# Kernel tuning notes

Hardware: AMD Instinct MI355X
Metric: run time of the kernel (lower is better)

The kernel has to match this reference:

```python
import jax, jax.numpy as jnp
import numpy as np

DIM = 512
QK_DIM = 128
B, N = 4, 4096
LN_EPS = 1e-5


def setup_inputs() -> dict:
    key = jax.random.key(0)
    ks = jax.random.split(key, 4)
    x = jax.random.normal(ks[0], (B, N, DIM), dtype=jnp.float32)
    ln_w = jnp.ones((DIM,), jnp.float32)
    ln_b = jnp.zeros((DIM,), jnp.float32)
    # Linear(dim -> qk_dim): torch default kaiming-uniform; small uniform is fine
    lim = 1.0 / np.sqrt(DIM)
    w_qk = jax.random.uniform(ks[1], (QK_DIM, DIM), jnp.float32, -lim, lim)
    b_qk = jax.random.uniform(ks[2], (QK_DIM,), jnp.float32, -lim, lim)
    # OffsetScale: gamma ~ N(0, 0.02), beta = 0, heads=2 (q, k)
    gamma = 0.02 * jax.random.normal(ks[3], (2, QK_DIM), jnp.float32)
    beta = jnp.zeros((2, QK_DIM), jnp.float32)
    return {"x": x, "ln_w": ln_w, "ln_b": ln_b, "w_qk": w_qk, "b_qk": b_qk, "gamma": gamma, "beta": beta}


def reference(x, ln_w, ln_b, w_qk, b_qk, gamma, beta):
    n = x.shape[-2]
    # LayerNorm over last dim
    mu = jnp.mean(x, axis=-1, keepdims=True)
    var = jnp.mean((x - mu) ** 2, axis=-1, keepdims=True)
    normed = (x - mu) * jax.lax.rsqrt(var + LN_EPS) * ln_w + ln_b
    # Linear + SiLU -> [b, n, qk_dim]
    qk = jax.nn.silu(jnp.einsum('bnd,ed->bne', normed, w_qk) + b_qk)
    # OffsetScale, heads=2 -> q, k
    q = qk * gamma[0] + beta[0]
    k = qk * gamma[1] + beta[1]
    # relu^2 row-normalized attention, [b, n, n]
    sim = jnp.einsum('bid,bjd->bij', q, k) / jnp.sqrt(jnp.float32(n))
    attn = jnp.square(jax.nn.relu(sim))
    attn = attn / (jnp.sum(attn, axis=-1, keepdims=True) + 1e-6)
    return attn
```

## Files before the change

### kernel.cpp

```cpp
#include <hip/hip_runtime.h>

#define DIM 512
#define QKD 128
#define BATCH 4
#define SEQ 4096

typedef __attribute__((ext_vector_type(8)))  _Float16 f16x8;
typedef __attribute__((ext_vector_type(4)))  _Float16 f16x4;
typedef __attribute__((ext_vector_type(4)))  float    f32x4;
typedef __attribute__((ext_vector_type(16))) float    f32x16;

__global__ __launch_bounds__(256) void wcvt_kernel(
    const float* __restrict__ w, _Float16* __restrict__ w16)
{
    const int i = (blockIdx.x * 256 + threadIdx.x) * 4;
    const float4 v = *(const float4*)(w + i);
    f16x4 o;
    o[0] = (_Float16)v.x; o[1] = (_Float16)v.y;
    o[2] = (_Float16)v.z; o[3] = (_Float16)v.w;
    *(f16x4*)(w16 + i) = o;
}

__global__ __launch_bounds__(256) void ln_qk_kernel(
    const float* __restrict__ x,
    const float* __restrict__ ln_w,
    const float* __restrict__ ln_b,
    const _Float16* __restrict__ w16,
    const float* __restrict__ b_qk,
    const float* __restrict__ gamma,
    const float* __restrict__ beta,
    _Float16* __restrict__ q_h,
    _Float16* __restrict__ k_h)
{
    __shared__ _Float16 As[32][520];
    const int tid  = threadIdx.x;
    const int wave = tid >> 6;
    const int lane = tid & 63;
    const int row0 = blockIdx.x * 32;

    float lw[8], lb[8];
    {
        const float4* w4 = (const float4*)ln_w;
        const float4* b4 = (const float4*)ln_b;
        float4 w0 = w4[lane * 2], w1 = w4[lane * 2 + 1];
        float4 b0 = b4[lane * 2], b1 = b4[lane * 2 + 1];
        lw[0]=w0.x; lw[1]=w0.y; lw[2]=w0.z; lw[3]=w0.w;
        lw[4]=w1.x; lw[5]=w1.y; lw[6]=w1.z; lw[7]=w1.w;
        lb[0]=b0.x; lb[1]=b0.y; lb[2]=b0.z; lb[3]=b0.w;
        lb[4]=b1.x; lb[5]=b1.y; lb[6]=b1.z; lb[7]=b1.w;
    }

    for (int rr = 0; rr < 8; ++rr) {
        const int r = wave * 8 + rr;
        const float4* xr = (const float4*)(x + (size_t)(row0 + r) * DIM);
        float4 v0 = xr[lane * 2], v1 = xr[lane * 2 + 1];
        float xv[8] = {v0.x, v0.y, v0.z, v0.w, v1.x, v1.y, v1.z, v1.w};
        float s = 0.f, s2 = 0.f;
#pragma unroll
        for (int j = 0; j < 8; ++j) { s += xv[j]; s2 = fmaf(xv[j], xv[j], s2); }
#pragma unroll
        for (int off = 32; off > 0; off >>= 1) {
            s  += __shfl_xor(s,  off);
            s2 += __shfl_xor(s2, off);
        }
        const float mu   = s * (1.f / DIM);
        const float var  = s2 * (1.f / DIM) - mu * mu;
        const float rstd = rsqrtf(var + 1e-5f);
        f16x8 hh;
#pragma unroll
        for (int j = 0; j < 8; ++j)
            hh[j] = (_Float16)(fmaf((xv[j] - mu) * rstd, lw[j], lb[j]));
        *(f16x8*)&As[r][lane * 8] = hh;
    }
    __syncthreads();

    const int mtile = wave & 1;
    const int nbase = (wave >> 1) * 64;
    const int lcol  = lane & 15;
    const int quad  = lane >> 4;

    f32x4 acc[4];
#pragma unroll
    for (int nt = 0; nt < 4; ++nt) acc[nt] = (f32x4){0.f, 0.f, 0.f, 0.f};

    const _Float16* arow = &As[mtile * 16 + lcol][quad * 8];
#pragma unroll 4
    for (int kc = 0; kc < 16; ++kc) {
        const f16x8 af = *(const f16x8*)(arow + kc * 32);
#pragma unroll
        for (int nt = 0; nt < 4; ++nt) {
            const int e = nbase + nt * 16 + lcol;
            const f16x8 bfr = *(const f16x8*)(w16 + (size_t)e * DIM + kc * 32 + quad * 8);
            acc[nt] = __builtin_amdgcn_mfma_f32_16x16x32_f16(af, bfr, acc[nt], 0, 0, 0);
        }
    }

#pragma unroll
    for (int nt = 0; nt < 4; ++nt) {
        const int e = nbase + nt * 16 + lcol;
        const float bq  = b_qk[e];
        const float g0  = gamma[e]       * 0.125f;
        const float g1  = gamma[QKD + e] * 0.125f;
        const float be0 = beta[e]        * 0.125f;
        const float be1 = beta[QKD + e]  * 0.125f;
#pragma unroll
        for (int reg = 0; reg < 4; ++reg) {
            const int m  = mtile * 16 + quad * 4 + reg;
            const float v   = acc[nt][reg] + bq;
            const float sil = v / (1.f + __expf(-v));
            const size_t off = (size_t)(row0 + m) * QKD + e;
            q_h[off] = (_Float16)fmaf(sil, g0, be0);
            k_h[off] = (_Float16)fmaf(sil, g1, be1);
        }
    }
}

__global__ __launch_bounds__(256, 3) void attn_kernel(
    const _Float16* __restrict__ q_h,
    const _Float16* __restrict__ k_h,
    float* __restrict__ out)
{
    const int l     = blockIdx.x;
    const int batch = (l & 7) >> 1;
    const int tile  = ((l >> 3) << 1) | (l & 1);
    const int r0    = tile * 32;

    const int wid  = threadIdx.x >> 6;
    const int lane = threadIdx.x & 63;
    const int n    = lane & 31;
    const int h    = lane >> 5;

    const _Float16* qb = q_h + ((size_t)batch * SEQ + r0) * QKD;
    f16x8 aq[8];
#pragma unroll
    for (int kc = 0; kc < 8; ++kc)
        aq[kc] = *(const f16x8*)(qb + (size_t)n * QKD + kc * 16 + h * 8);

    const _Float16* kb = k_h + (size_t)batch * SEQ * QKD
                             + (size_t)(wid * 32 + n) * QKD + h * 8;

    __shared__ float partial[4][32];
    __shared__ float srow_s[32];

    float rs[16];
#pragma unroll
    for (int r = 0; r < 16; ++r) rs[r] = 0.f;

#pragma unroll 2
    for (int ct = 0; ct < 32; ++ct) {
        const _Float16* cb = kb + (size_t)(ct * 128) * QKD;
        f16x8 bf[8];
#pragma unroll
        for (int kc = 0; kc < 8; ++kc) bf[kc] = *(const f16x8*)(cb + kc * 16);

        f32x16 acc;
#pragma unroll
        for (int r = 0; r < 16; ++r) acc[r] = 0.f;
#pragma unroll
        for (int kc = 0; kc < 8; ++kc)
            acc = __builtin_amdgcn_mfma_f32_32x32x16_f16(aq[kc], bf[kc], acc, 0, 0, 0);
#pragma unroll
        for (int r = 0; r < 16; ++r) {
            const float t = fmaxf(acc[r], 0.f);
            rs[r] = fmaf(t, t, rs[r]);
        }
    }

#pragma unroll
    for (int r = 0; r < 16; ++r) {
        float v = rs[r];
        v += __shfl_xor(v, 1);
        v += __shfl_xor(v, 2);
        v += __shfl_xor(v, 4);
        v += __shfl_xor(v, 8);
        v += __shfl_xor(v, 16);
        if (n == 0) partial[wid][(r & 3) + 8 * (r >> 2) + 4 * h] = v;
    }
    __syncthreads();
    if (threadIdx.x < 32) {
        const float t = partial[0][threadIdx.x] + partial[1][threadIdx.x]
                      + partial[2][threadIdx.x] + partial[3][threadIdx.x];
        srow_s[threadIdx.x] = rsqrtf(t + 1e-6f);
    }
    __syncthreads();

    float srow[16];
#pragma unroll
    for (int r = 0; r < 16; ++r)
        srow[r] = srow_s[(r & 3) + 8 * (r >> 2) + 4 * h];

    float* ob = out + ((size_t)batch * SEQ + r0) * SEQ;

#pragma unroll 2
    for (int ct = 0; ct < 32; ++ct) {
        const _Float16* cb = kb + (size_t)(ct * 128) * QKD;
        f16x8 bf[8];
#pragma unroll
        for (int kc = 0; kc < 8; ++kc) bf[kc] = *(const f16x8*)(cb + kc * 16);

        f32x16 acc;
#pragma unroll
        for (int r = 0; r < 16; ++r) acc[r] = 0.f;
#pragma unroll
        for (int kc = 0; kc < 8; ++kc)
            acc = __builtin_amdgcn_mfma_f32_32x32x16_f16(aq[kc], bf[kc], acc, 0, 0, 0);

        const int col = ct * 128 + wid * 32 + n;
#pragma unroll
        for (int r = 0; r < 16; ++r) {
            const float t   = fmaxf(acc[r], 0.f) * srow[r];
            const int   row = (r & 3) + 8 * (r >> 2) + 4 * h;
            __builtin_nontemporal_store(t * t, ob + (size_t)row * SEQ + col);
        }
    }
}

extern "C" void kernel_launch(void* const* d_in, const int* in_sizes, int n_in,
                              void* d_out, int out_size, void* d_ws, size_t ws_size,
                              hipStream_t stream) {
    const float* x     = (const float*)d_in[0];
    const float* ln_w  = (const float*)d_in[1];
    const float* ln_b  = (const float*)d_in[2];
    const float* w_qk  = (const float*)d_in[3];
    const float* b_qk  = (const float*)d_in[4];
    const float* gamma = (const float*)d_in[5];
    const float* beta  = (const float*)d_in[6];
    float* out = (float*)d_out;

    _Float16* q_h = (_Float16*)d_ws;
    _Float16* k_h = q_h + (size_t)BATCH * SEQ * QKD;
    _Float16* w16 = k_h + (size_t)BATCH * SEQ * QKD;

    hipLaunchKernelGGL(wcvt_kernel, dim3(64), dim3(256), 0, stream, w_qk, w16);
    hipLaunchKernelGGL(ln_qk_kernel, dim3((BATCH * SEQ) / 32), dim3(256), 0, stream,
                       x, ln_w, ln_b, w16, b_qk, gamma, beta, q_h, k_h);
    hipLaunchKernelGGL(attn_kernel, dim3(BATCH * (SEQ / 32)), dim3(256), 0, stream,
                       q_h, k_h, out);
}
```

Measured before the change: 397.9 us.

## Split attention into separate row-sum and normalize kernels over column chunks

The fused attention kernel, which computed row sums and then recomputed and wrote the output, becomes two kernels. Each kernel splits the 4096 columns into four chunks of 1024, so there are 2048 blocks instead of 512. The first kernel writes partial row sums to workspace and the second combines them before normalizing and storing. The aim is more parallelism and occupancy (launch bound raised to 4). It also raises wave priority around the MFMA sequences. The cost is an extra launch, an extra round trip through global memory, and more repeated Q loads.

Result: slower. 410.4 us (+3.1%).

```diff
diff --git a/kernel.cpp b/kernel.cpp
--- a/kernel.cpp
+++ b/kernel.cpp
@@ -115,15 +115,17 @@
     }
 }
 
-__global__ __launch_bounds__(256, 3) void attn_kernel(
+__global__ __launch_bounds__(256, 4) void rowsum_kernel(
     const _Float16* __restrict__ q_h,
     const _Float16* __restrict__ k_h,
-    float* __restrict__ out)
+    float* __restrict__ rsum)
 {
     const int l     = blockIdx.x;
     const int batch = (l & 7) >> 1;
-    const int tile  = ((l >> 3) << 1) | (l & 1);
+    const int chunk = ((l & 1) << 1) | ((l >> 3) & 1);
+    const int tile  = l >> 4;
     const int r0    = tile * 32;
+    const int c0    = chunk * 1024;
 
     const int wid  = threadIdx.x >> 6;
     const int lane = threadIdx.x & 63;
@@ -137,17 +139,16 @@
         aq[kc] = *(const f16x8*)(qb + (size_t)n * QKD + kc * 16 + h * 8);
 
     const _Float16* kb = k_h + (size_t)batch * SEQ * QKD
-                             + (size_t)(wid * 32 + n) * QKD + h * 8;
+                             + (size_t)(c0 + wid * 32 + n) * QKD + h * 8;
 
     __shared__ float partial[4][32];
-    __shared__ float srow_s[32];
 
     float rs[16];
 #pragma unroll
     for (int r = 0; r < 16; ++r) rs[r] = 0.f;
 
 #pragma unroll 2
-    for (int ct = 0; ct < 32; ++ct) {
+    for (int ct = 0; ct < 8; ++ct) {
         const _Float16* cb = kb + (size_t)(ct * 128) * QKD;
         f16x8 bf[8];
 #pragma unroll
@@ -156,9 +157,11 @@
         f32x16 acc;
 #pragma unroll
         for (int r = 0; r < 16; ++r) acc[r] = 0.f;
+        __builtin_amdgcn_s_setprio(1);
 #pragma unroll
         for (int kc = 0; kc < 8; ++kc)
             acc = __builtin_amdgcn_mfma_f32_32x32x16_f16(aq[kc], bf[kc], acc, 0, 0, 0);
+        __builtin_amdgcn_s_setprio(0);
 #pragma unroll
         for (int r = 0; r < 16; ++r) {
             const float t = fmaxf(acc[r], 0.f);
@@ -180,6 +183,39 @@
     if (threadIdx.x < 32) {
         const float t = partial[0][threadIdx.x] + partial[1][threadIdx.x]
                       + partial[2][threadIdx.x] + partial[3][threadIdx.x];
+        rsum[((size_t)batch * 4 + chunk) * SEQ + r0 + threadIdx.x] = t;
+    }
+}
+
+__global__ __launch_bounds__(256, 4) void attn_norm_kernel(
+    const _Float16* __restrict__ q_h,
+    const _Float16* __restrict__ k_h,
+    const float* __restrict__ rsum,
+    float* __restrict__ out)
+{
+    const int l     = blockIdx.x;
+    const int batch = (l & 7) >> 1;
+    const int chunk = ((l & 1) << 1) | ((l >> 3) & 1);
+    const int tile  = l >> 4;
+    const int r0    = tile * 32;
+    const int c0    = chunk * 1024;
+
+    const int wid  = threadIdx.x >> 6;
+    const int lane = threadIdx.x & 63;
+    const int n    = lane & 31;
+    const int h    = lane >> 5;
+
+    const _Float16* qb = q_h + ((size_t)batch * SEQ + r0) * QKD;
+    f16x8 aq[8];
+#pragma unroll
+    for (int kc = 0; kc < 8; ++kc)
+        aq[kc] = *(const f16x8*)(qb + (size_t)n * QKD + kc * 16 + h * 8);
+
+    __shared__ float srow_s[32];
+    if (threadIdx.x < 32) {
+        const size_t base = (size_t)batch * 4 * SEQ + r0 + threadIdx.x;
+        const float t = rsum[base] + rsum[base + SEQ]
+                      + rsum[base + 2 * SEQ] + rsum[base + 3 * SEQ];
         srow_s[threadIdx.x] = rsqrtf(t + 1e-6f);
     }
     __syncthreads();
@@ -189,10 +225,12 @@
     for (int r = 0; r < 16; ++r)
         srow[r] = srow_s[(r & 3) + 8 * (r >> 2) + 4 * h];
 
+    const _Float16* kb = k_h + (size_t)batch * SEQ * QKD
+                             + (size_t)(c0 + wid * 32 + n) * QKD + h * 8;
     float* ob = out + ((size_t)batch * SEQ + r0) * SEQ;
 
 #pragma unroll 2
-    for (int ct = 0; ct < 32; ++ct) {
+    for (int ct = 0; ct < 8; ++ct) {
         const _Float16* cb = kb + (size_t)(ct * 128) * QKD;
         f16x8 bf[8];
 #pragma unroll
@@ -201,11 +239,13 @@
         f32x16 acc;
 #pragma unroll
         for (int r = 0; r < 16; ++r) acc[r] = 0.f;
+        __builtin_amdgcn_s_setprio(1);
 #pragma unroll
         for (int kc = 0; kc < 8; ++kc)
             acc = __builtin_amdgcn_mfma_f32_32x32x16_f16(aq[kc], bf[kc], acc, 0, 0, 0);
-
-        const int col = ct * 128 + wid * 32 + n;
+        __builtin_amdgcn_s_setprio(0);
+
+        const int col = c0 + ct * 128 + wid * 32 + n;
 #pragma unroll
         for (int r = 0; r < 16; ++r) {
             const float t   = fmaxf(acc[r], 0.f) * srow[r];
@@ -230,10 +270,13 @@
     _Float16* q_h = (_Float16*)d_ws;
     _Float16* k_h = q_h + (size_t)BATCH * SEQ * QKD;
     _Float16* w16 = k_h + (size_t)BATCH * SEQ * QKD;
+    float*    rsum = (float*)(w16 + (size_t)QKD * DIM);
 
     hipLaunchKernelGGL(wcvt_kernel, dim3(64), dim3(256), 0, stream, w_qk, w16);
     hipLaunchKernelGGL(ln_qk_kernel, dim3((BATCH * SEQ) / 32), dim3(256), 0, stream,
                        x, ln_w, ln_b, w16, b_qk, gamma, beta, q_h, k_h);
-    hipLaunchKernelGGL(attn_kernel, dim3(BATCH * (SEQ / 32)), dim3(256), 0, stream,
-                       q_h, k_h, out);
-}
+    hipLaunchKernelGGL(rowsum_kernel, dim3(2048), dim3(256), 0, stream,
+                       q_h, k_h, rsum);
+    hipLaunchKernelGGL(attn_norm_kernel, dim3(2048), dim3(256), 0, stream,
+                       q_h, k_h, rsum, out);
+}
```

## Store Q/K and weights in MFMA fragment order, widen attention blocks to eight waves

Applied to the files above, without the earlier changes.

The weight conversion now writes W in MFMA B-fragment order, and the LN+QK kernel works on 16-row tiles, staging Q/K through shared memory so they are stored in a 32-row fragment-packed layout. This lets the attention kernel load operands as fully contiguous per-lane vectors. The attention kernel moves to 512 threads (8 waves covering 256 columns per step) and raises wave priority around the MFMA chains. Costs: extra LDS staging and sync in the projection kernel, and higher register pressure from the tighter launch bounds.

New measurement: 329.2 us, median of 2. 1.21x faster.

```diff
diff --git a/kernel.cpp b/kernel.cpp
--- a/kernel.cpp
+++ b/kernel.cpp
@@ -11,32 +11,42 @@
 typedef __attribute__((ext_vector_type(16))) float    f32x16;
 
 __global__ __launch_bounds__(256) void wcvt_kernel(
-    const float* __restrict__ w, _Float16* __restrict__ w16)
+    const float* __restrict__ w, _Float16* __restrict__ w16f)
 {
-    const int i = (blockIdx.x * 256 + threadIdx.x) * 4;
-    const float4 v = *(const float4*)(w + i);
-    f16x4 o;
-    o[0] = (_Float16)v.x; o[1] = (_Float16)v.y;
-    o[2] = (_Float16)v.z; o[3] = (_Float16)v.w;
-    *(f16x4*)(w16 + i) = o;
-}
-
-__global__ __launch_bounds__(256) void ln_qk_kernel(
+    const int t    = blockIdx.x * 256 + threadIdx.x;
+    const int lane = t & 63;
+    const int nb   = (t >> 6) & 7;
+    const int kc   = t >> 9;
+    const int e    = nb * 16 + (lane & 15);
+    const int d0   = kc * 32 + (lane >> 4) * 8;
+    const float4* src = (const float4*)(w + (size_t)e * DIM + d0);
+    const float4 a = src[0], b = src[1];
+    f16x8 o;
+    o[0] = (_Float16)a.x; o[1] = (_Float16)a.y;
+    o[2] = (_Float16)a.z; o[3] = (_Float16)a.w;
+    o[4] = (_Float16)b.x; o[5] = (_Float16)b.y;
+    o[6] = (_Float16)b.z; o[7] = (_Float16)b.w;
+    *(f16x8*)(w16f + (size_t)t * 8) = o;
+}
+
+__global__ __launch_bounds__(256, 4) void ln_qk_kernel(
     const float* __restrict__ x,
     const float* __restrict__ ln_w,
     const float* __restrict__ ln_b,
-    const _Float16* __restrict__ w16,
+    const _Float16* __restrict__ w16f,
     const float* __restrict__ b_qk,
     const float* __restrict__ gamma,
     const float* __restrict__ beta,
     _Float16* __restrict__ q_h,
     _Float16* __restrict__ k_h)
 {
-    __shared__ _Float16 As[32][520];
+    __shared__ _Float16 As[16][520];
+    __shared__ _Float16 Qs[16][136];
+    __shared__ _Float16 Ks[16][136];
     const int tid  = threadIdx.x;
     const int wave = tid >> 6;
     const int lane = tid & 63;
-    const int row0 = blockIdx.x * 32;
+    const int row0 = blockIdx.x * 16;
 
     float lw[8], lb[8];
     {
@@ -50,11 +60,17 @@
         lb[4]=b1.x; lb[5]=b1.y; lb[6]=b1.z; lb[7]=b1.w;
     }
 
-    for (int rr = 0; rr < 8; ++rr) {
-        const int r = wave * 8 + rr;
-        const float4* xr = (const float4*)(x + (size_t)(row0 + r) * DIM);
-        float4 v0 = xr[lane * 2], v1 = xr[lane * 2 + 1];
-        float xv[8] = {v0.x, v0.y, v0.z, v0.w, v1.x, v1.y, v1.z, v1.w};
+    float4 xa[4], xb[4];
+#pragma unroll
+    for (int rr = 0; rr < 4; ++rr) {
+        const float4* xr = (const float4*)(x + (size_t)(row0 + wave * 4 + rr) * DIM);
+        xa[rr] = xr[lane * 2];
+        xb[rr] = xr[lane * 2 + 1];
+    }
+#pragma unroll
+    for (int rr = 0; rr < 4; ++rr) {
+        float xv[8] = {xa[rr].x, xa[rr].y, xa[rr].z, xa[rr].w,
+                       xb[rr].x, xb[rr].y, xb[rr].z, xb[rr].w};
         float s = 0.f, s2 = 0.f;
 #pragma unroll
         for (int j = 0; j < 8; ++j) { s += xv[j]; s2 = fmaf(xv[j], xv[j], s2); }
@@ -70,34 +86,32 @@
 #pragma unroll
         for (int j = 0; j < 8; ++j)
             hh[j] = (_Float16)(fmaf((xv[j] - mu) * rstd, lw[j], lb[j]));
-        *(f16x8*)&As[r][lane * 8] = hh;
-    }
-    __syncthreads();
-
-    const int mtile = wave & 1;
-    const int nbase = (wave >> 1) * 64;
-    const int lcol  = lane & 15;
-    const int quad  = lane >> 4;
-
-    f32x4 acc[4];
-#pragma unroll
-    for (int nt = 0; nt < 4; ++nt) acc[nt] = (f32x4){0.f, 0.f, 0.f, 0.f};
-
-    const _Float16* arow = &As[mtile * 16 + lcol][quad * 8];
+        *(f16x8*)&As[wave * 4 + rr][lane * 8] = hh;
+    }
+    __syncthreads();
+
+    const int lcol = lane & 15;
+    const int quad = lane >> 4;
+
+    f32x4 acc[2];
+    acc[0] = (f32x4){0.f, 0.f, 0.f, 0.f};
+    acc[1] = (f32x4){0.f, 0.f, 0.f, 0.f};
+
+    const _Float16* arow = &As[lcol][quad * 8];
 #pragma unroll 4
     for (int kc = 0; kc < 16; ++kc) {
         const f16x8 af = *(const f16x8*)(arow + kc * 32);
 #pragma unroll
-        for (int nt = 0; nt < 4; ++nt) {
-            const int e = nbase + nt * 16 + lcol;
-            const f16x8 bfr = *(const f16x8*)(w16 + (size_t)e * DIM + kc * 32 + quad * 8);
+        for (int nt = 0; nt < 2; ++nt) {
+            const f16x8 bfr = *(const f16x8*)(
+                w16f + (size_t)((kc * 8 + wave * 2 + nt) * 64 + lane) * 8);
             acc[nt] = __builtin_amdgcn_mfma_f32_16x16x32_f16(af, bfr, acc[nt], 0, 0, 0);
         }
     }
 
 #pragma unroll
-    for (int nt = 0; nt < 4; ++nt) {
-        const int e = nbase + nt * 16 + lcol;
+    for (int nt = 0; nt < 2; ++nt) {
+        const int e = (wave * 2 + nt) * 16 + lcol;
         const float bq  = b_qk[e];
         const float g0  = gamma[e]       * 0.125f;
         const float g1  = gamma[QKD + e] * 0.125f;
@@ -105,17 +119,27 @@
         const float be1 = beta[QKD + e]  * 0.125f;
 #pragma unroll
         for (int reg = 0; reg < 4; ++reg) {
-            const int m  = mtile * 16 + quad * 4 + reg;
+            const int m  = quad * 4 + reg;
             const float v   = acc[nt][reg] + bq;
             const float sil = v / (1.f + __expf(-v));
-            const size_t off = (size_t)(row0 + m) * QKD + e;
-            q_h[off] = (_Float16)fmaf(sil, g0, be0);
-            k_h[off] = (_Float16)fmaf(sil, g1, be1);
-        }
-    }
-}
-
-__global__ __launch_bounds__(256, 3) void attn_kernel(
+            Qs[m][e] = (_Float16)fmaf(sil, g0, be0);
+            Ks[m][e] = (_Float16)fmaf(sil, g1, be1);
+        }
+    }
+    __syncthreads();
+
+    {
+        const int mm = tid & 15, eh = tid >> 4;
+        const f16x8 qv = *(const f16x8*)&Qs[mm][eh * 8];
+        const f16x8 kv = *(const f16x8*)&Ks[mm][eh * 8];
+        const size_t base = ((size_t)(blockIdx.x >> 1)) * 4096
+                          + (size_t)eh * 256 + (blockIdx.x & 1) * 128 + mm * 8;
+        *(f16x8*)(q_h + base) = qv;
+        *(f16x8*)(k_h + base) = kv;
+    }
+}
+
+__global__ __launch_bounds__(512, 4) void attn_kernel(
     const _Float16* __restrict__ q_h,
     const _Float16* __restrict__ k_h,
     float* __restrict__ out)
@@ -123,23 +147,21 @@
     const int l     = blockIdx.x;
     const int batch = (l & 7) >> 1;
     const int tile  = ((l >> 3) << 1) | (l & 1);
-    const int r0    = tile * 32;
 
     const int wid  = threadIdx.x >> 6;
     const int lane = threadIdx.x & 63;
     const int n    = lane & 31;
     const int h    = lane >> 5;
 
-    const _Float16* qb = q_h + ((size_t)batch * SEQ + r0) * QKD;
+    const _Float16* qb = q_h + (size_t)(batch * 128 + tile) * 4096;
     f16x8 aq[8];
 #pragma unroll
     for (int kc = 0; kc < 8; ++kc)
-        aq[kc] = *(const f16x8*)(qb + (size_t)n * QKD + kc * 16 + h * 8);
-
-    const _Float16* kb = k_h + (size_t)batch * SEQ * QKD
-                             + (size_t)(wid * 32 + n) * QKD + h * 8;
-
-    __shared__ float partial[4][32];
+        aq[kc] = *(const f16x8*)(qb + kc * 512 + lane * 8);
+
+    const _Float16* kb0 = k_h + (size_t)(batch * 128 + wid) * 4096 + lane * 8;
+
+    __shared__ float partial[8][32];
     __shared__ float srow_s[32];
 
     float rs[16];
@@ -147,18 +169,20 @@
     for (int r = 0; r < 16; ++r) rs[r] = 0.f;
 
 #pragma unroll 2
-    for (int ct = 0; ct < 32; ++ct) {
-        const _Float16* cb = kb + (size_t)(ct * 128) * QKD;
+    for (int ct = 0; ct < 16; ++ct) {
+        const _Float16* cb = kb0 + (size_t)(ct * 8) * 4096;
         f16x8 bf[8];
 #pragma unroll
-        for (int kc = 0; kc < 8; ++kc) bf[kc] = *(const f16x8*)(cb + kc * 16);
+        for (int kc = 0; kc < 8; ++kc) bf[kc] = *(const f16x8*)(cb + kc * 512);
 
         f32x16 acc;
 #pragma unroll
         for (int r = 0; r < 16; ++r) acc[r] = 0.f;
+        __builtin_amdgcn_s_setprio(1);
 #pragma unroll
         for (int kc = 0; kc < 8; ++kc)
             acc = __builtin_amdgcn_mfma_f32_32x32x16_f16(aq[kc], bf[kc], acc, 0, 0, 0);
+        __builtin_amdgcn_s_setprio(0);
 #pragma unroll
         for (int r = 0; r < 16; ++r) {
             const float t = fmaxf(acc[r], 0.f);
@@ -178,8 +202,9 @@
     }
     __syncthreads();
     if (threadIdx.x < 32) {
-        const float t = partial[0][threadIdx.x] + partial[1][threadIdx.x]
-                      + partial[2][threadIdx.x] + partial[3][threadIdx.x];
+        float t = 0.f;
+#pragma unroll
+        for (int w = 0; w < 8; ++w) t += partial[w][threadIdx.x];
         srow_s[threadIdx.x] = rsqrtf(t + 1e-6f);
     }
     __syncthreads();
@@ -189,23 +214,25 @@
     for (int r = 0; r < 16; ++r)
         srow[r] = srow_s[(r & 3) + 8 * (r >> 2) + 4 * h];
 
-    float* ob = out + ((size_t)batch * SEQ + r0) * SEQ;
+    float* ob = out + ((size_t)batch * SEQ + tile * 32) * SEQ;
 
 #pragma unroll 2
-    for (int ct = 0; ct < 32; ++ct) {
-        const _Float16* cb = kb + (size_t)(ct * 128) * QKD;
+    for (int ct = 0; ct < 16; ++ct) {
+        const _Float16* cb = kb0 + (size_t)(ct * 8) * 4096;
         f16x8 bf[8];
 #pragma unroll
-        for (int kc = 0; kc < 8; ++kc) bf[kc] = *(const f16x8*)(cb + kc * 16);
+        for (int kc = 0; kc < 8; ++kc) bf[kc] = *(const f16x8*)(cb + kc * 512);
 
         f32x16 acc;
 #pragma unroll
         for (int r = 0; r < 16; ++r) acc[r] = 0.f;
+        __builtin_amdgcn_s_setprio(1);
 #pragma unroll
         for (int kc = 0; kc < 8; ++kc)
             acc = __builtin_amdgcn_mfma_f32_32x32x16_f16(aq[kc], bf[kc], acc, 0, 0, 0);
-
-        const int col = ct * 128 + wid * 32 + n;
+        __builtin_amdgcn_s_setprio(0);
+
+        const int col = ct * 256 + wid * 32 + n;
 #pragma unroll
         for (int r = 0; r < 16; ++r) {
             const float t   = fmaxf(acc[r], 0.f) * srow[r];
@@ -227,13 +254,13 @@
     const float* beta  = (const float*)d_in[6];
     float* out = (float*)d_out;
 
-    _Float16* q_h = (_Float16*)d_ws;
-    _Float16* k_h = q_h + (size_t)BATCH * SEQ * QKD;
-    _Float16* w16 = k_h + (size_t)BATCH * SEQ * QKD;
-
-    hipLaunchKernelGGL(wcvt_kernel, dim3(64), dim3(256), 0, stream, w_qk, w16);
-    hipLaunchKernelGGL(ln_qk_kernel, dim3((BATCH * SEQ) / 32), dim3(256), 0, stream,
-                       x, ln_w, ln_b, w16, b_qk, gamma, beta, q_h, k_h);
-    hipLaunchKernelGGL(attn_kernel, dim3(BATCH * (SEQ / 32)), dim3(256), 0, stream,
+    _Float16* q_h  = (_Float16*)d_ws;
+    _Float16* k_h  = q_h + (size_t)BATCH * SEQ * QKD;
+    _Float16* w16f = k_h + (size_t)BATCH * SEQ * QKD;
+
+    hipLaunchKernelGGL(wcvt_kernel, dim3(32), dim3(256), 0, stream, w_qk, w16f);
+    hipLaunchKernelGGL(ln_qk_kernel, dim3((BATCH * SEQ) / 16), dim3(256), 0, stream,
+                       x, ln_w, ln_b, w16f, b_qk, gamma, beta, q_h, k_h);
+    hipLaunchKernelGGL(attn_kernel, dim3(BATCH * (SEQ / 32)), dim3(512), 0, stream,
                        q_h, k_h, out);
 }
```
